# Kernel optimization log

Hardware: AMD Instinct MI355X
Metric: run time of the kernel (lower is better)

Reference implementation:

```python
import jax, jax.numpy as jnp
import numpy as np

BN_EPS = 1e-5


def setup_inputs() -> dict:
    key = jax.random.key(0)
    ks = jax.random.split(key, 8)
    B, C, H, W = 2, 512, 64, 64
    Ck, Cv = 256, 256
    x = jax.random.normal(ks[0], (B, C, H, W), jnp.float32)
    # f_key/f_query shared 1x1 conv (kaiming, relu)
    wk = jax.random.normal(ks[1], (Ck, C), jnp.float32) * (2.0 / C) ** 0.5
    bk = jnp.zeros((Ck,), jnp.float32)
    bn_gamma = jax.random.uniform(ks[2], (Ck,), jnp.float32, 0.5, 1.5)
    bn_beta = jax.random.normal(ks[3], (Ck,), jnp.float32) * 0.1
    bn_mean = jax.random.normal(ks[4], (Ck,), jnp.float32) * 0.1
    bn_var = jax.random.uniform(ks[5], (Ck,), jnp.float32, 0.5, 1.5)
    # f_value: 3x3 conv then 1x1 conv
    wv1 = jax.random.normal(ks[6], (Cv, C, 3, 3), jnp.float32) * (2.0 / (C * 9)) ** 0.5
    bv1 = jnp.zeros((Cv,), jnp.float32)
    wv2 = jax.random.normal(ks[7], (Cv, Cv), jnp.float32) * (2.0 / Cv) ** 0.5
    bv2 = jnp.zeros((Cv,), jnp.float32)
    return dict(x=x, wk=wk, bk=bk, bn_gamma=bn_gamma, bn_beta=bn_beta,
                bn_mean=bn_mean, bn_var=bn_var, wv1=wv1, bv1=bv1, wv2=wv2, bv2=bv2)


def reference(x, wk, bk, bn_gamma, bn_beta, bn_mean, bn_var, wv1, bv1, wv2, bv2):
    B, C, H, W = x.shape
    Ck, Cv = wk.shape[0], wv1.shape[0]
    N = H * W
    # f_key == f_query: 1x1 conv + BN (inference form) + ReLU
    feat = jnp.einsum('oc,bchw->bohw', wk, x) + bk[:, None, None]
    scale_bn = (bn_gamma / jnp.sqrt(bn_var + BN_EPS))
    feat = (feat - bn_mean[:, None, None]) * scale_bn[:, None, None] + bn_beta[:, None, None]
    feat = jax.nn.relu(feat).reshape(B, Ck, N)  # [B, Ck, N]
    # sim_map = softmax(Ck^-0.5 * Q^T K); Q and K are the same tensor
    sim_map = jax.nn.softmax(jnp.einsum('bcn,bcm->bnm', feat, feat) * (Ck ** -0.5), axis=-1)
    # f_value: conv3x3 + relu + conv1x1 + relu
    v = jax.lax.conv_general_dilated(x, wv1, (1, 1), 'SAME',
                                     dimension_numbers=('NCHW', 'OIHW', 'NCHW'))
    v = jax.nn.relu(v + bv1[:, None, None])
    v = jax.nn.relu(jnp.einsum('oc,bchw->bohw', wv2, v) + bv2[:, None, None])
    v = v.reshape(B, Cv, N)  # [B, Cv, N]
    context = jnp.einsum('bnm,bcm->bcn', sim_map, v).reshape(B, Cv, H, W)
    return context, sim_map
```

## Files before the change

### kernel.cpp

```cpp
#include <hip/hip_runtime.h>
#include <hip/hip_bf16.h>
#include <stdint.h>

typedef unsigned short u16_t;
typedef __attribute__((ext_vector_type(8))) short short8;
typedef __attribute__((ext_vector_type(4))) float f32x4;
typedef __attribute__((ext_vector_type(4))) unsigned short us4;

__device__ __forceinline__ float bf2f(u16_t u) {
  union { unsigned int i; float f; } c; c.i = ((unsigned int)u) << 16; return c.f;
}
__device__ __forceinline__ u16_t f2bf(float f) {
  union { float f; unsigned int i; } c; c.f = f;
  unsigned int x = c.i;
  unsigned int r = x + 0x7fffu + ((x >> 16) & 1u);
  return (u16_t)(r >> 16);
}

__device__ __forceinline__ void gload_lds16(const u16_t* g, u16_t* l) {
  __builtin_amdgcn_global_load_lds(
      (const __attribute__((address_space(1))) void*)g,
      (__attribute__((address_space(3))) void*)(unsigned int)(uintptr_t)l,
      16, 0, 0);
}

struct Seg {
  const u16_t* Ah;
  const u16_t* Al;
  const u16_t* Bh;
  const u16_t* Bl;
  int boff;
};

struct GemmArgs {
  Seg segs[9];
  int nseg;
  int segs_per_split;
  int K;
  int ldA, ldB;
  long long sA, sB;
  float alpha;
  float* outf;
  long long sOut;
  long long sSplit;
  int ldT;
};

template<int BM, int BN, int MODE, bool PADB, bool SYMM, int NCH = 4>
__global__ __launch_bounds__(256, 4) void gemm_tn(GemmArgs args) {
  constexpr int FM = BM / 32, FN = BN / 32;
  constexpr int AH_E = NCH * BM * 8;
  constexpr int AL_E = (MODE == 0) ? NCH * BM * 8 : 8;
  constexpr int BH_E = NCH * BN * 8;
  constexpr int BL_E = (MODE <= 1) ? NCH * BN * 8 : 8;
  constexpr int SM_E = AH_E + AL_E + BH_E + BL_E;
  static_assert(!SYMM || (size_t)SM_E * 2 >= 32 * 132 * 4, "tbuf alias too small");
  __shared__ __align__(16) u16_t smem[SM_E];
  u16_t* aflat_h = smem;
  u16_t* aflat_l = smem + AH_E;
  u16_t* bflat_h = smem + AH_E + AL_E;
  u16_t* bflat_l = smem + AH_E + AL_E + BH_E;

  const int tid = threadIdx.x;
  const int wave = tid >> 6, lane = tid & 63;
  const int lhi = lane >> 4, llo = lane & 15;
  const int wr = wave >> 1, wc = wave & 1;
  int nt, mt, b, split;
  if (SYMM) {
    b = blockIdx.z; split = 0;
    int t = blockIdx.x, r = 0;
    while (t >= 32 - r) { t -= 32 - r; ++r; }
    mt = r; nt = r + t;
  } else {
    nt = blockIdx.x; mt = blockIdx.y;
    b = blockIdx.z & 1; split = blockIdx.z >> 1;
  }
  const int row0 = mt * BM, col0 = nt * BN;

  f32x4 acc[FM][FN];
  const f32x4 zero4 = {0.f, 0.f, 0.f, 0.f};
#pragma unroll
  for (int i = 0; i < FM; ++i)
#pragma unroll
    for (int j = 0; j < FN; ++j) acc[i][j] = zero4;

  constexpr int RA = BM * NCH / 256;
  constexpr int RB = BN * NCH / 256;

  const int s0 = split * args.segs_per_split;
  int s1 = s0 + args.segs_per_split;
  if (s1 > args.nseg) s1 = args.nseg;

  for (int s = s0; s < s1; ++s) {
    const u16_t* Abh = args.segs[s].Ah + (size_t)b * args.sA;
    const u16_t* Abl = args.segs[s].Al + (size_t)b * args.sA;
    const u16_t* Bbh = args.segs[s].Bh + (size_t)b * args.sB;
    const u16_t* Bbl = args.segs[s].Bl + (size_t)b * args.sB;
    const int boff = args.segs[s].boff;
    for (int k0 = 0; k0 < args.K; k0 += NCH * 8) {
      __syncthreads();
#pragma unroll
      for (int r = 0; r < RA; ++r) {
        int idx = r * 256 + tid;
        int chunk = idx / BM, m = idx % BM;
        size_t goff = (size_t)(row0 + m) * args.ldA + (k0 + chunk * 8);
        gload_lds16(Abh + goff, aflat_h + (size_t)idx * 8);
        if (MODE == 0)
          gload_lds16(Abl + goff, aflat_l + (size_t)idx * 8);
      }
#pragma unroll
      for (int r = 0; r < RB; ++r) {
        int idx = r * 256 + tid;
        int chunk = idx / BN, n = idx % BN;
        long long rowi;
        if (PADB) {
          int gn = col0 + n;
          rowi = (long long)((gn >> 6) + 1) * 66 + (gn & 63) + 1 + boff;
        } else {
          rowi = col0 + n;
        }
        size_t goff = (size_t)rowi * args.ldB + (k0 + chunk * 8);
        gload_lds16(Bbh + goff, bflat_h + (size_t)idx * 8);
        if (MODE <= 1)
          gload_lds16(Bbl + goff, bflat_l + (size_t)idx * 8);
      }
      __syncthreads();
#pragma unroll
      for (int kk = 0; kk < NCH / 4; ++kk) {
        const int ckA = (kk * 4 + lhi) * BM;
        const int ckB = (kk * 4 + lhi) * BN;
        short8 afh[FM], afl[FM], bfh[FN], bfl[FN];
#pragma unroll
        for (int i = 0; i < FM; ++i) {
          afh[i] = *(const short8*)(aflat_h + ((size_t)ckA + wr * (BM / 2) + i * 16 + llo) * 8);
          if (MODE == 0)
            afl[i] = *(const short8*)(aflat_l + ((size_t)ckA + wr * (BM / 2) + i * 16 + llo) * 8);
        }
#pragma unroll
        for (int j = 0; j < FN; ++j) {
          bfh[j] = *(const short8*)(bflat_h + ((size_t)ckB + wc * (BN / 2) + j * 16 + llo) * 8);
          if (MODE <= 1)
            bfl[j] = *(const short8*)(bflat_l + ((size_t)ckB + wc * (BN / 2) + j * 16 + llo) * 8);
        }
#pragma unroll
        for (int i = 0; i < FM; ++i)
#pragma unroll
          for (int j = 0; j < FN; ++j) {
            f32x4 t = acc[i][j];
            if (MODE <= 1)
              t = __builtin_amdgcn_mfma_f32_16x16x32_bf16(afh[i], bfl[j], t, 0, 0, 0);
            if (MODE == 0)
              t = __builtin_amdgcn_mfma_f32_16x16x32_bf16(afl[i], bfh[j], t, 0, 0, 0);
            t = __builtin_amdgcn_mfma_f32_16x16x32_bf16(afh[i], bfh[j], t, 0, 0, 0);
            acc[i][j] = t;
          }
      }
    }
  }

  float* outp = args.outf + (size_t)split * args.sSplit + (size_t)b * args.sOut;
#pragma unroll
  for (int i = 0; i < FM; ++i) {
    int mb = row0 + wr * (BM / 2) + i * 16 + lhi * 4;
#pragma unroll
    for (int j = 0; j < FN; ++j) {
      int n = col0 + wc * (BN / 2) + j * 16 + llo;
      f32x4 vv = acc[i][j] * args.alpha;
      *(f32x4*)(outp + (size_t)n * args.ldT + mb) = vv;
    }
  }
  if (SYMM) {
    if (nt != mt) {
      float* tb = (float*)smem;
#pragma unroll
      for (int i = 0; i < FM; ++i) {
        __syncthreads();
#pragma unroll
        for (int j = 0; j < FN; ++j) {
#pragma unroll
          for (int r2 = 0; r2 < 4; ++r2) {
            int trow = wr * 16 + lhi * 4 + r2;
            int tcol = wc * 64 + j * 16 + llo;
            tb[trow * 132 + tcol] = acc[i][j][r2] * args.alpha;
          }
        }
        __syncthreads();
#pragma unroll
        for (int it = 0; it < 4; ++it) {
          int idx = it * 256 + tid;
          int row = idx >> 5, c4 = idx & 31;
          int mg = row0 + (row >> 4) * 64 + i * 16 + (row & 15);
          f32x4 v4 = *(f32x4*)&tb[row * 132 + c4 * 4];
          *(f32x4*)(outp + (size_t)mg * args.ldT + col0 + c4 * 4) = v4;
        }
      }
    }
  }
}

struct Conv3Args {
  const u16_t* W;
  const u16_t* X;
  float* outf;
  long long sOut;
  long long sSplit;
};
__global__ __launch_bounds__(256, 4) void conv3_gemm(Conv3Args a) {
  __shared__ __align__(16) u16_t lA[3][4][128][8];
  __shared__ __align__(16) u16_t lB[4 * 144 * 8];
  const int tid = threadIdx.x;
  const int wave = tid >> 6, lane = tid & 63;
  const int lhi = lane >> 4, llo = lane & 15;
  const int wr = wave >> 1, wc = wave & 1;
  const int nt = blockIdx.x, mt = blockIdx.y;
  const int z = blockIdx.z;
  const int b = z & 1;
  const int rest = z >> 1;
  const int ty = rest % 3, kh = rest / 3;
  const int row0 = mt * 128;
  const int base = (2 * nt + ty) * 66;
  const u16_t* Xb = a.X + (size_t)b * 4356 * 512;
  const u16_t* Wt = a.W + (size_t)(ty * 3) * 131072;

  f32x4 acc[4][4];
  const f32x4 zero4 = {0.f, 0.f, 0.f, 0.f};
#pragma unroll
  for (int i = 0; i < 4; ++i)
#pragma unroll
    for (int j = 0; j < 4; ++j) acc[i][j] = zero4;

  for (int k0 = kh * 256; k0 < (kh + 1) * 256; k0 += 32) {
    __syncthreads();
#pragma unroll
    for (int t = 0; t < 3; ++t)
#pragma unroll
      for (int r = 0; r < 2; ++r) {
        int slot = r * 256 + tid;
        int chunk = slot >> 7, m = slot & 127;
        const u16_t* src = Wt + (size_t)t * 131072 + (size_t)(row0 + m) * 512 + k0 + chunk * 8;
        gload_lds16(src, &lA[t][0][0][0] + (size_t)slot * 8);
      }
#pragma unroll
    for (int r = 0; r < 2; ++r) {
      int idx = r * 256 + tid;
      int chunk = idx / 144, rr = idx % 144;
      gload_lds16(Xb + (size_t)(base + rr) * 512 + k0 + chunk * 8, lB + (size_t)idx * 8);
    }
    if (tid < 64) {
      int idx = 512 + tid;
      int chunk = idx / 144, rr = idx % 144;
      gload_lds16(Xb + (size_t)(base + rr) * 512 + k0 + chunk * 8, lB + (size_t)idx * 8);
    }
    __syncthreads();
#pragma unroll
    for (int t = 0; t < 3; ++t) {
      short8 af[4], bf[4];
#pragma unroll
      for (int i = 0; i < 4; ++i)
        af[i] = *(const short8*)&lA[t][lhi][wr * 64 + i * 16 + llo][0];
#pragma unroll
      for (int j = 0; j < 4; ++j) {
        int rB = wc * 66 + j * 16 + llo + t;
        bf[j] = *(const short8*)(lB + ((size_t)lhi * 144 + rB) * 8);
      }
#pragma unroll
      for (int i = 0; i < 4; ++i)
#pragma unroll
        for (int j = 0; j < 4; ++j)
          acc[i][j] = __builtin_amdgcn_mfma_f32_16x16x32_bf16(af[i], bf[j], acc[i][j], 0, 0, 0);
    }
  }

  float* outp = a.outf + (size_t)(ty + 3 * kh) * a.sSplit + (size_t)b * a.sOut;
#pragma unroll
  for (int i = 0; i < 4; ++i) {
    int mb = row0 + wr * 64 + i * 16 + lhi * 4;
#pragma unroll
    for (int j = 0; j < 4; ++j) {
      int n = (nt << 7) + wc * 64 + j * 16 + llo;
      *(f32x4*)(outp + (size_t)n * 256 + mb) = acc[i][j];
    }
  }
}

template<int LDT, bool PER_COL>
__global__ __launch_bounds__(256) void reduce_split(
    const float* __restrict__ part, long long sSplit, int ns,
    const float* __restrict__ scale, const float* __restrict__ bias,
    u16_t* __restrict__ oh, u16_t* __restrict__ ol, long long total) {
  long long i = ((long long)blockIdx.x * 256 + threadIdx.x) * 4;
  if (i >= total) return;
  f32x4 s = *(const f32x4*)(part + i);
  for (int p = 1; p < ns; ++p) s += *(const f32x4*)(part + (size_t)p * sSplit + i);
  f32x4 v;
  if (PER_COL) {
    int c = (int)(i & (LDT - 1));
    f32x4 bi = *(const f32x4*)(bias + c);
    if (scale) { f32x4 sc = *(const f32x4*)(scale + c); v = s * sc + bi; }
    else v = s + bi;
  } else {
    int r = (int)((i / LDT) & 255);
    float bi = bias[r];
    v = s + bi;
  }
  us4 h, l;
#pragma unroll
  for (int c2 = 0; c2 < 4; ++c2) {
    float vv = v[c2] > 0.f ? v[c2] : 0.f;
    u16_t hh = f2bf(vv);
    h[c2] = hh;
    l[c2] = f2bf(vv - bf2f(hh));
  }
  *(us4*)(oh + i) = h;
  if (ol) *(us4*)(ol + i) = l;
}

__global__ __launch_bounds__(256) void reduce_split_f32(
    const float* __restrict__ part, long long sSplit, int ns,
    float* __restrict__ out, long long total) {
  long long i = ((long long)blockIdx.x * 256 + threadIdx.x) * 4;
  if (i >= total) return;
  f32x4 s = *(const f32x4*)(part + i);
  for (int p = 1; p < ns; ++p) s += *(const f32x4*)(part + (size_t)p * sSplit + i);
  __builtin_nontemporal_store(s, (f32x4*)(out + i));
}

__global__ __launch_bounds__(256) void softmax_k(float* S, u16_t* P) {
  const int row = blockIdx.x;
  float* Sr = S + (size_t)row * 4096;
  u16_t* Pr = P + (size_t)row * 4096;
  const int t = threadIdx.x;
  const int wave = t >> 6;
  f32x4 v[4];
  float vmax = -3.4e38f;
#pragma unroll
  for (int i = 0; i < 4; ++i) {
    v[i] = ((const f32x4*)Sr)[t + i * 256];
#pragma unroll
    for (int c = 0; c < 4; ++c) vmax = fmaxf(vmax, v[i][c]);
  }
#pragma unroll
  for (int off = 32; off; off >>= 1) vmax = fmaxf(vmax, __shfl_xor(vmax, off));
  __shared__ float red[4];
  if ((t & 63) == 0) red[wave] = vmax;
  __syncthreads();
  vmax = fmaxf(fmaxf(red[0], red[1]), fmaxf(red[2], red[3]));
  float sum = 0.f;
#pragma unroll
  for (int i = 0; i < 4; ++i)
#pragma unroll
    for (int c = 0; c < 4; ++c) { v[i][c] = __expf(v[i][c] - vmax); sum += v[i][c]; }
#pragma unroll
  for (int off = 32; off; off >>= 1) sum += __shfl_xor(sum, off);
  __shared__ float red2[4];
  if ((t & 63) == 0) red2[wave] = sum;
  __syncthreads();
  sum = red2[0] + red2[1] + red2[2] + red2[3];
  float rs = 1.0f / sum;
#pragma unroll
  for (int i = 0; i < 4; ++i) {
    f32x4 o = v[i] * rs;
    __builtin_nontemporal_store(o, (f32x4*)Sr + t + i * 256);
    us4 pb;
#pragma unroll
    for (int c = 0; c < 4; ++c) pb[c] = f2bf(o[c]);
    ((us4*)Pr)[t + i * 256] = pb;
  }
}

__global__ __launch_bounds__(256) void xprep(const float* __restrict__ x,
                                             u16_t* __restrict__ xh, u16_t* __restrict__ xl) {
  __shared__ float tile[64][65];
  const int b = blockIdx.z, c0 = blockIdx.y * 64, n0 = blockIdx.x * 64;
  const float* xb = x + ((size_t)b * 512 + c0) * 4096 + n0;
  const int t = threadIdx.x;
  const int tr = t >> 6, tc = t & 63;
#pragma unroll
  for (int rr = 0; rr < 16; ++rr) {
    int ci = tr + rr * 4;
    tile[ci][tc] = xb[(size_t)ci * 4096 + tc];
  }
  __syncthreads();
#pragma unroll
  for (int rr = 0; rr < 16; ++rr) {
    int nj = rr * 4 + tr;
    float v = tile[tc][nj];
    size_t rp = (size_t)(blockIdx.x + 1) * 66 + nj + 1;
    size_t o = ((size_t)b * 4356 + rp) * 512 + c0 + tc;
    u16_t hh = f2bf(v);
    xh[o] = hh;
    xl[o] = f2bf(v - bf2f(hh));
  }
}

__global__ __launch_bounds__(256) void prep_all(
    const float* __restrict__ wk, const float* __restrict__ wv2, const float* __restrict__ wv1,
    const float* __restrict__ g, const float* __restrict__ be, const float* __restrict__ mu,
    const float* __restrict__ var, const float* __restrict__ bkb,
    u16_t* __restrict__ wkh, u16_t* __restrict__ wkl,
    u16_t* __restrict__ w2h, u16_t* __restrict__ w2l,
    u16_t* __restrict__ w1h, float* __restrict__ bnA, float* __restrict__ bnB,
    u16_t* __restrict__ xh, u16_t* __restrict__ xl) {
  long long i = (long long)blockIdx.x * 256 + threadIdx.x;
  if (i < 256) {
    float s = g[i] * rsqrtf(var[i] + 1e-5f);
    bnA[i] = s;
    bnB[i] = (bkb[i] - mu[i]) * s + be[i];
    return;
  }
  i -= 256;
  if (i < 131072) {
    float v = wk[i];
    u16_t hh = f2bf(v);
    wkh[i] = hh; wkl[i] = f2bf(v - bf2f(hh));
    return;
  }
  i -= 131072;
  if (i < 65536) {
    float v = wv2[i];
    u16_t hh = f2bf(v);
    w2h[i] = hh; w2l[i] = f2bf(v - bf2f(hh));
    return;
  }
  i -= 65536;
  if (i < 1179648) {
    int tp = (int)(i / (256 * 512));
    int rem = (int)(i % (256 * 512));
    int o = rem / 512, c = rem % 512;
    w1h[i] = f2bf(wv1[((size_t)o * 512 + c) * 9 + tp]);
    return;
  }
  i -= 1179648;
  if (i < 133120) {
    int blk = (int)(i >> 8), t = (int)(i & 255);
    int rowi = blk % 260, b = blk / 260;
    int rp;
    if (rowi < 66) rp = rowi;
    else if (rowi < 132) rp = 4290 + (rowi - 66);
    else { int g2 = (rowi - 132) >> 1; rp = (g2 + 1) * 66 + ((rowi - 132) & 1) * 65; }
    size_t base = ((size_t)b * 4356 + rp) * 512;
    const us4 z = {0, 0, 0, 0};
    if (t < 128) *(us4*)(xh + base + (size_t)t * 4) = z;
    else *(us4*)(xl + base + (size_t)(t - 128) * 4) = z;
  }
}

extern "C" void kernel_launch(void* const* d_in, const int* in_sizes, int n_in,
                              void* d_out, int out_size, void* d_ws, size_t ws_size,
                              hipStream_t stream) {
  (void)in_sizes; (void)n_in; (void)out_size; (void)ws_size;
  const float* x   = (const float*)d_in[0];
  const float* wk  = (const float*)d_in[1];
  const float* bk  = (const float*)d_in[2];
  const float* gam = (const float*)d_in[3];
  const float* bet = (const float*)d_in[4];
  const float* mu  = (const float*)d_in[5];
  const float* var = (const float*)d_in[6];
  const float* wv1 = (const float*)d_in[7];
  const float* bv1 = (const float*)d_in[8];
  const float* wv2 = (const float*)d_in[9];
  const float* bv2 = (const float*)d_in[10];

  const int B = 2;
  const size_t XT_E  = (size_t)B * 4356 * 512;
  const size_t WK_E  = 256 * 512;
  const size_t WV1_E = 9ull * 256 * 512;
  const size_t WV2_E = 256 * 256;
  const size_t FT_E  = (size_t)B * 4096 * 256;
  const size_t P_E   = (size_t)B * 4096 * 4096;

  size_t off = 0;
  auto carve = [&](size_t bytes) -> char* {
    off = (off + 255) & ~(size_t)255;
    char* p = (char*)d_ws + off;
    off += bytes;
    return p;
  };
  u16_t* xh  = (u16_t*)carve(XT_E * 2);
  u16_t* xl  = (u16_t*)carve(XT_E * 2);
  u16_t* wkh = (u16_t*)carve(WK_E * 2);
  u16_t* wkl = (u16_t*)carve(WK_E * 2);
  u16_t* w1h = (u16_t*)carve(WV1_E * 2);
  u16_t* w2h = (u16_t*)carve(WV2_E * 2);
  u16_t* w2l = (u16_t*)carve(WV2_E * 2);
  u16_t* fth = (u16_t*)carve(FT_E * 2);
  u16_t* ftl = (u16_t*)carve(FT_E * 2);
  u16_t* v1h = (u16_t*)carve(FT_E * 2);
  u16_t* v1l = (u16_t*)carve(FT_E * 2);
  u16_t* vh  = (u16_t*)carve(FT_E * 2);
  u16_t* Pb  = (u16_t*)carve(P_E * 2);
  float* bnA = (float*)carve(256 * 4);
  float* bnB = (float*)carve(256 * 4);

  float* big_part = (float*)Pb;
  float* pv_part  = (float*)d_ws;

  float* ctx = (float*)d_out;
  float* sim = (float*)d_out + (size_t)B * 256 * 4096;

  const long long FT_LL = (long long)FT_E;

  prep_all<<<5897, 256, 0, stream>>>(wk, wv2, wv1, gam, bet, mu, var, bk,
                                     wkh, wkl, w2h, w2l, w1h, bnA, bnB, xh, xl);
  xprep<<<dim3(64, 8, 2), 256, 0, stream>>>(x, xh, xl);

  {
    GemmArgs a = {};
    a.segs[0] = {wkh,       wkl,       xh,       xl,       0};
    a.segs[1] = {wkh + 256, wkl + 256, xh + 256, xl + 256, 0};
    a.nseg = 2; a.segs_per_split = 1; a.K = 256; a.ldA = 512; a.ldB = 512;
    a.sA = 0; a.sB = (long long)4356 * 512; a.alpha = 1.f;
    a.outf = big_part; a.sOut = (long long)4096 * 256; a.sSplit = FT_LL; a.ldT = 256;
    gemm_tn<64, 128, 0, true, false><<<dim3(32, 4, 4), 256, 0, stream>>>(a);
    reduce_split<256, true><<<2048, 256, 0, stream>>>(big_part, FT_LL, 2, bnA, bnB, fth, ftl, FT_LL);
  }
  {
    GemmArgs a = {};
    a.segs[0] = {fth, nullptr, fth, ftl, 0};
    a.nseg = 1; a.segs_per_split = 1; a.K = 256; a.ldA = 256; a.ldB = 256;
    a.sA = (long long)4096 * 256; a.sB = (long long)4096 * 256; a.alpha = 0.0625f;
    a.outf = sim; a.sOut = (long long)4096 * 4096; a.sSplit = 0; a.ldT = 4096;
    gemm_tn<128, 128, 1, false, true><<<dim3(528, 1, 2), 256, 0, stream>>>(a);
  }
  {
    Conv3Args a;
    a.W = w1h; a.X = xh;
    a.outf = big_part; a.sOut = (long long)4096 * 256; a.sSplit = FT_LL;
    conv3_gemm<<<dim3(32, 2, 12), 256, 0, stream>>>(a);
    reduce_split<256, true><<<2048, 256, 0, stream>>>(big_part, FT_LL, 6, nullptr, bv1, v1h, v1l, FT_LL);
  }
  {
    GemmArgs a = {};
    a.segs[0] = {v1h,       v1l,       w2h,       w2l,       0};
    a.segs[1] = {v1h + 128, v1l + 128, w2h + 128, w2l + 128, 0};
    a.nseg = 2; a.segs_per_split = 1; a.K = 128; a.ldA = 256; a.ldB = 256;
    a.sA = (long long)4096 * 256; a.sB = 0; a.alpha = 1.f;
    a.outf = big_part; a.sOut = (long long)256 * 4096; a.sSplit = FT_LL; a.ldT = 4096;
    gemm_tn<128, 64, 0, false, false><<<dim3(4, 32, 4), 256, 0, stream>>>(a);
    reduce_split<4096, false><<<2048, 256, 0, stream>>>(big_part, FT_LL, 2, nullptr, bv2, vh, nullptr, FT_LL);
  }
  softmax_k<<<B * 4096, 256, 0, stream>>>(sim, Pb);
  {
    GemmArgs a = {};
    for (int q = 0; q < 4; ++q)
      a.segs[q] = {Pb + (size_t)q * 1024, nullptr, vh + (size_t)q * 1024, nullptr, 0};
    a.nseg = 4; a.segs_per_split = 1; a.K = 1024; a.ldA = 4096; a.ldB = 4096;
    a.sA = (long long)4096 * 4096; a.sB = (long long)256 * 4096; a.alpha = 1.f;
    a.outf = pv_part; a.sOut = (long long)256 * 4096; a.sSplit = FT_LL; a.ldT = 4096;
    gemm_tn<128, 128, 2, false, false, 8><<<dim3(2, 32, 8), 256, 0, stream>>>(a);
    reduce_split_f32<<<2048, 256, 0, stream>>>(pv_part, FT_LL, 4, ctx, FT_LL);
  }
}
```

Measured before the change: 265.7 us.

## Co-schedule independent QK/conv3 and wv2/softmax work in fused interleaved kernels

```diff
diff --git a/kernel.cpp b/kernel.cpp
--- a/kernel.cpp
+++ b/kernel.cpp
@@ -46,7 +46,7 @@
   int ldT;
 };
 
-template<int BM, int BN, int MODE, bool PADB, bool SYMM, int NCH = 4>
+template<int BM, int BN, int MODE, bool PADB, int NCH = 4>
 __global__ __launch_bounds__(256, 4) void gemm_tn(GemmArgs args) {
   constexpr int FM = BM / 32, FN = BN / 32;
   constexpr int AH_E = NCH * BM * 8;
@@ -54,7 +54,6 @@
   constexpr int BH_E = NCH * BN * 8;
   constexpr int BL_E = (MODE <= 1) ? NCH * BN * 8 : 8;
   constexpr int SM_E = AH_E + AL_E + BH_E + BL_E;
-  static_assert(!SYMM || (size_t)SM_E * 2 >= 32 * 132 * 4, "tbuf alias too small");
   __shared__ __align__(16) u16_t smem[SM_E];
   u16_t* aflat_h = smem;
   u16_t* aflat_l = smem + AH_E;
@@ -65,16 +64,8 @@
   const int wave = tid >> 6, lane = tid & 63;
   const int lhi = lane >> 4, llo = lane & 15;
   const int wr = wave >> 1, wc = wave & 1;
-  int nt, mt, b, split;
-  if (SYMM) {
-    b = blockIdx.z; split = 0;
-    int t = blockIdx.x, r = 0;
-    while (t >= 32 - r) { t -= 32 - r; ++r; }
-    mt = r; nt = r + t;
-  } else {
-    nt = blockIdx.x; mt = blockIdx.y;
-    b = blockIdx.z & 1; split = blockIdx.z >> 1;
-  }
+  const int nt = blockIdx.x, mt = blockIdx.y;
+  const int b = blockIdx.z & 1, split = blockIdx.z >> 1;
   const int row0 = mt * BM, col0 = nt * BN;
 
   f32x4 acc[FM][FN];
@@ -169,19 +160,101 @@
       *(f32x4*)(outp + (size_t)n * args.ldT + mb) = vv;
     }
   }
-  if (SYMM) {
+}
+
+struct QkConvArgs {
+  const u16_t* fh;
+  const u16_t* fl;
+  float* sim;
+  const u16_t* W;
+  const u16_t* X;
+  float* cpart;
+  long long sOut;
+  long long sSplit;
+};
+__global__ __launch_bounds__(256, 4) void qk_conv_fused(QkConvArgs a) {
+  __shared__ __align__(16) u16_t smem[16896];
+  const int tid = threadIdx.x;
+  const int wave = tid >> 6, lane = tid & 63;
+  const int lhi = lane >> 4, llo = lane & 15;
+  const int wr = wave >> 1, wc = wave & 1;
+  const int bid = blockIdx.x;
+  const int grp = bid / 19, r19 = bid % 19;
+
+  if (r19 < 11) {
+    int id = grp * 11 + r19;
+    int b = id / 528;
+    int t = id % 528, rr_ = 0;
+    while (t >= 32 - rr_) { t -= 32 - rr_; ++rr_; }
+    const int mt = rr_, nt = rr_ + t;
+    const int row0 = mt * 128, col0 = nt * 128;
+    u16_t* aflat_h = smem;
+    u16_t* bflat_h = smem + 4096;
+    u16_t* bflat_l = smem + 8192;
+    const u16_t* Fh = a.fh + (size_t)b * 4096 * 256;
+    const u16_t* Fl = a.fl + (size_t)b * 4096 * 256;
+
+    f32x4 acc[4][4];
+    const f32x4 zero4 = {0.f, 0.f, 0.f, 0.f};
+#pragma unroll
+    for (int i = 0; i < 4; ++i)
+#pragma unroll
+      for (int j = 0; j < 4; ++j) acc[i][j] = zero4;
+
+    for (int k0 = 0; k0 < 256; k0 += 32) {
+      __syncthreads();
+#pragma unroll
+      for (int rr = 0; rr < 2; ++rr) {
+        int idx = rr * 256 + tid;
+        int chunk = idx >> 7, m = idx & 127;
+        gload_lds16(Fh + (size_t)(row0 + m) * 256 + k0 + chunk * 8, aflat_h + (size_t)idx * 8);
+        gload_lds16(Fh + (size_t)(col0 + m) * 256 + k0 + chunk * 8, bflat_h + (size_t)idx * 8);
+        gload_lds16(Fl + (size_t)(col0 + m) * 256 + k0 + chunk * 8, bflat_l + (size_t)idx * 8);
+      }
+      __syncthreads();
+      short8 afh[4], bfh[4], bfl[4];
+#pragma unroll
+      for (int i = 0; i < 4; ++i)
+        afh[i] = *(const short8*)(aflat_h + ((size_t)lhi * 128 + wr * 64 + i * 16 + llo) * 8);
+#pragma unroll
+      for (int j = 0; j < 4; ++j) {
+        bfh[j] = *(const short8*)(bflat_h + ((size_t)lhi * 128 + wc * 64 + j * 16 + llo) * 8);
+        bfl[j] = *(const short8*)(bflat_l + ((size_t)lhi * 128 + wc * 64 + j * 16 + llo) * 8);
+      }
+#pragma unroll
+      for (int i = 0; i < 4; ++i)
+#pragma unroll
+        for (int j = 0; j < 4; ++j) {
+          f32x4 tt = acc[i][j];
+          tt = __builtin_amdgcn_mfma_f32_16x16x32_bf16(afh[i], bfl[j], tt, 0, 0, 0);
+          tt = __builtin_amdgcn_mfma_f32_16x16x32_bf16(afh[i], bfh[j], tt, 0, 0, 0);
+          acc[i][j] = tt;
+        }
+    }
+
+    float* outp = a.sim + (size_t)b * 4096 * 4096;
+#pragma unroll
+    for (int i = 0; i < 4; ++i) {
+      int mb = row0 + wr * 64 + i * 16 + lhi * 4;
+#pragma unroll
+      for (int j = 0; j < 4; ++j) {
+        int n = col0 + wc * 64 + j * 16 + llo;
+        f32x4 vv = acc[i][j] * 0.0625f;
+        *(f32x4*)(outp + (size_t)n * 4096 + mb) = vv;
+      }
+    }
     if (nt != mt) {
       float* tb = (float*)smem;
 #pragma unroll
-      for (int i = 0; i < FM; ++i) {
+      for (int i = 0; i < 4; ++i) {
         __syncthreads();
 #pragma unroll
-        for (int j = 0; j < FN; ++j) {
+        for (int j = 0; j < 4; ++j) {
 #pragma unroll
           for (int r2 = 0; r2 < 4; ++r2) {
             int trow = wr * 16 + lhi * 4 + r2;
             int tcol = wc * 64 + j * 16 + llo;
-            tb[trow * 132 + tcol] = acc[i][j][r2] * args.alpha;
+            tb[trow * 132 + tcol] = acc[i][j][r2] * 0.0625f;
           }
         }
         __syncthreads();
@@ -191,94 +264,221 @@
           int row = idx >> 5, c4 = idx & 31;
           int mg = row0 + (row >> 4) * 64 + i * 16 + (row & 15);
           f32x4 v4 = *(f32x4*)&tb[row * 132 + c4 * 4];
-          *(f32x4*)(outp + (size_t)mg * args.ldT + col0 + c4 * 4) = v4;
-        }
-      }
-    }
-  }
-}
-
-struct Conv3Args {
-  const u16_t* W;
-  const u16_t* X;
-  float* outf;
+          *(f32x4*)(outp + (size_t)mg * 4096 + col0 + c4 * 4) = v4;
+        }
+      }
+    }
+  } else {
+    int id = grp * 8 + (r19 - 11);
+    const int nt = id & 31;
+    const int mt = (id >> 5) & 1;
+    const int z = id >> 6;
+    const int b = z & 1;
+    const int rest = z >> 1;
+    const int ty = rest % 3, kh = rest / 3;
+    const int row0 = mt * 128;
+    const int base = (2 * nt + ty) * 66;
+    const u16_t* Xb = a.X + (size_t)b * 4356 * 512;
+    const u16_t* Wt = a.W + (size_t)(ty * 3) * 131072;
+    u16_t* lA = smem;
+    u16_t* lB = smem + 12288;
+
+    f32x4 acc[4][4];
+    const f32x4 zero4 = {0.f, 0.f, 0.f, 0.f};
+#pragma unroll
+    for (int i = 0; i < 4; ++i)
+#pragma unroll
+      for (int j = 0; j < 4; ++j) acc[i][j] = zero4;
+
+    for (int k0 = kh * 256; k0 < (kh + 1) * 256; k0 += 32) {
+      __syncthreads();
+#pragma unroll
+      for (int t = 0; t < 3; ++t)
+#pragma unroll
+        for (int r = 0; r < 2; ++r) {
+          int slot = r * 256 + tid;
+          int chunk = slot >> 7, m = slot & 127;
+          const u16_t* src = Wt + (size_t)t * 131072 + (size_t)(row0 + m) * 512 + k0 + chunk * 8;
+          gload_lds16(src, lA + (size_t)t * 4096 + (size_t)slot * 8);
+        }
+#pragma unroll
+      for (int r = 0; r < 2; ++r) {
+        int idx = r * 256 + tid;
+        int chunk = idx / 144, rr = idx % 144;
+        gload_lds16(Xb + (size_t)(base + rr) * 512 + k0 + chunk * 8, lB + (size_t)idx * 8);
+      }
+      if (tid < 64) {
+        int idx = 512 + tid;
+        int chunk = idx / 144, rr = idx % 144;
+        gload_lds16(Xb + (size_t)(base + rr) * 512 + k0 + chunk * 8, lB + (size_t)idx * 8);
+      }
+      __syncthreads();
+#pragma unroll
+      for (int t = 0; t < 3; ++t) {
+        short8 af[4], bf[4];
+#pragma unroll
+        for (int i = 0; i < 4; ++i)
+          af[i] = *(const short8*)(lA + (size_t)t * 4096 + ((size_t)lhi * 128 + wr * 64 + i * 16 + llo) * 8);
+#pragma unroll
+        for (int j = 0; j < 4; ++j) {
+          int rB = wc * 66 + j * 16 + llo + t;
+          bf[j] = *(const short8*)(lB + ((size_t)lhi * 144 + rB) * 8);
+        }
+#pragma unroll
+        for (int i = 0; i < 4; ++i)
+#pragma unroll
+          for (int j = 0; j < 4; ++j)
+            acc[i][j] = __builtin_amdgcn_mfma_f32_16x16x32_bf16(af[i], bf[j], acc[i][j], 0, 0, 0);
+      }
+    }
+
+    float* outp = a.cpart + (size_t)(ty + 3 * kh) * a.sSplit + (size_t)b * a.sOut;
+#pragma unroll
+    for (int i = 0; i < 4; ++i) {
+      int mb = row0 + wr * 64 + i * 16 + lhi * 4;
+#pragma unroll
+      for (int j = 0; j < 4; ++j) {
+        int n = (nt << 7) + wc * 64 + j * 16 + llo;
+        *(f32x4*)(outp + (size_t)n * 256 + mb) = acc[i][j];
+      }
+    }
+  }
+}
+
+struct Wv2SmArgs {
+  const u16_t* v1h;
+  const u16_t* v1l;
+  const u16_t* w2h;
+  const u16_t* w2l;
+  float* wpart;
   long long sOut;
   long long sSplit;
+  float* S;
+  u16_t* P;
 };
-__global__ __launch_bounds__(256, 4) void conv3_gemm(Conv3Args a) {
-  __shared__ __align__(16) u16_t lA[3][4][128][8];
-  __shared__ __align__(16) u16_t lB[4 * 144 * 8];
+__global__ __launch_bounds__(256, 4) void wv2_softmax_fused(Wv2SmArgs a) {
+  __shared__ __align__(16) u16_t smem[12288];
   const int tid = threadIdx.x;
-  const int wave = tid >> 6, lane = tid & 63;
-  const int lhi = lane >> 4, llo = lane & 15;
-  const int wr = wave >> 1, wc = wave & 1;
-  const int nt = blockIdx.x, mt = blockIdx.y;
-  const int z = blockIdx.z;
-  const int b = z & 1;
-  const int rest = z >> 1;
-  const int ty = rest % 3, kh = rest / 3;
-  const int row0 = mt * 128;
-  const int base = (2 * nt + ty) * 66;
-  const u16_t* Xb = a.X + (size_t)b * 4356 * 512;
-  const u16_t* Wt = a.W + (size_t)(ty * 3) * 131072;
-
-  f32x4 acc[4][4];
-  const f32x4 zero4 = {0.f, 0.f, 0.f, 0.f};
-#pragma unroll
-  for (int i = 0; i < 4; ++i)
-#pragma unroll
-    for (int j = 0; j < 4; ++j) acc[i][j] = zero4;
-
-  for (int k0 = kh * 256; k0 < (kh + 1) * 256; k0 += 32) {
+  const int bid = blockIdx.x;
+  const int grp = bid / 17, r17 = bid % 17;
+
+  if (r17 == 0) {
+    const int id = grp;
+    const int wave = tid >> 6, lane = tid & 63;
+    const int lhi = lane >> 4, llo = lane & 15;
+    const int wr = wave >> 1, wc = wave & 1;
+    const int nt = id & 3;
+    const int mt = (id >> 2) & 31;
+    const int z = id >> 7;
+    const int b = z & 1, split = z >> 1;
+    const int row0 = mt * 128, col0 = nt * 64;
+    u16_t* aflat_h = smem;
+    u16_t* aflat_l = smem + 4096;
+    u16_t* bflat_h = smem + 8192;
+    u16_t* bflat_l = smem + 10240;
+    const u16_t* Abh = a.v1h + (size_t)b * 4096 * 256 + split * 128;
+    const u16_t* Abl = a.v1l + (size_t)b * 4096 * 256 + split * 128;
+    const u16_t* Bbh = a.w2h + split * 128;
+    const u16_t* Bbl = a.w2l + split * 128;
+
+    f32x4 acc[4][2];
+    const f32x4 zero4 = {0.f, 0.f, 0.f, 0.f};
+#pragma unroll
+    for (int i = 0; i < 4; ++i)
+#pragma unroll
+      for (int j = 0; j < 2; ++j) acc[i][j] = zero4;
+
+    for (int k0 = 0; k0 < 128; k0 += 32) {
+      __syncthreads();
+#pragma unroll
+      for (int r = 0; r < 2; ++r) {
+        int idx = r * 256 + tid;
+        int chunk = idx >> 7, m = idx & 127;
+        size_t goff = (size_t)(row0 + m) * 256 + (k0 + chunk * 8);
+        gload_lds16(Abh + goff, aflat_h + (size_t)idx * 8);
+        gload_lds16(Abl + goff, aflat_l + (size_t)idx * 8);
+      }
+      {
+        int idx = tid;
+        int chunk = idx >> 6, n = idx & 63;
+        size_t goff = (size_t)(col0 + n) * 256 + (k0 + chunk * 8);
+        gload_lds16(Bbh + goff, bflat_h + (size_t)idx * 8);
+        gload_lds16(Bbl + goff, bflat_l + (size_t)idx * 8);
+      }
+      __syncthreads();
+      short8 afh[4], afl[4], bfh[2], bfl[2];
+#pragma unroll
+      for (int i = 0; i < 4; ++i) {
+        afh[i] = *(const short8*)(aflat_h + ((size_t)lhi * 128 + wr * 64 + i * 16 + llo) * 8);
+        afl[i] = *(const short8*)(aflat_l + ((size_t)lhi * 128 + wr * 64 + i * 16 + llo) * 8);
+      }
+#pragma unroll
+      for (int j = 0; j < 2; ++j) {
+        bfh[j] = *(const short8*)(bflat_h + ((size_t)lhi * 64 + wc * 32 + j * 16 + llo) * 8);
+        bfl[j] = *(const short8*)(bflat_l + ((size_t)lhi * 64 + wc * 32 + j * 16 + llo) * 8);
+      }
+#pragma unroll
+      for (int i = 0; i < 4; ++i)
+#pragma unroll
+        for (int j = 0; j < 2; ++j) {
+          f32x4 t = acc[i][j];
+          t = __builtin_amdgcn_mfma_f32_16x16x32_bf16(afh[i], bfl[j], t, 0, 0, 0);
+          t = __builtin_amdgcn_mfma_f32_16x16x32_bf16(afl[i], bfh[j], t, 0, 0, 0);
+          t = __builtin_amdgcn_mfma_f32_16x16x32_bf16(afh[i], bfh[j], t, 0, 0, 0);
+          acc[i][j] = t;
+        }
+    }
+
+    float* outp = a.wpart + (size_t)split * a.sSplit + (size_t)b * a.sOut;
+#pragma unroll
+    for (int i = 0; i < 4; ++i) {
+      int mb = row0 + wr * 64 + i * 16 + lhi * 4;
+#pragma unroll
+      for (int j = 0; j < 2; ++j) {
+        int n = col0 + wc * 32 + j * 16 + llo;
+        *(f32x4*)(outp + (size_t)n * 4096 + mb) = acc[i][j];
+      }
+    }
+  } else {
+    const int row = grp * 16 + (r17 - 1);
+    float* Sr = a.S + (size_t)row * 4096;
+    u16_t* Pr = a.P + (size_t)row * 4096;
+    const int t = tid;
+    const int wave = t >> 6;
+    float* red = (float*)smem;
+    float* red2 = red + 4;
+    f32x4 v[4];
+    float vmax = -3.4e38f;
+#pragma unroll
+    for (int i = 0; i < 4; ++i) {
+      v[i] = ((const f32x4*)Sr)[t + i * 256];
+#pragma unroll
+      for (int c = 0; c < 4; ++c) vmax = fmaxf(vmax, v[i][c]);
+    }
+#pragma unroll
+    for (int off = 32; off; off >>= 1) vmax = fmaxf(vmax, __shfl_xor(vmax, off));
+    if ((t & 63) == 0) red[wave] = vmax;
     __syncthreads();
-#pragma unroll
-    for (int t = 0; t < 3; ++t)
-#pragma unroll
-      for (int r = 0; r < 2; ++r) {
-        int slot = r * 256 + tid;
-        int chunk = slot >> 7, m = slot & 127;
-        const u16_t* src = Wt + (size_t)t * 131072 + (size_t)(row0 + m) * 512 + k0 + chunk * 8;
-        gload_lds16(src, &lA[t][0][0][0] + (size_t)slot * 8);
-      }
-#pragma unroll
-    for (int r = 0; r < 2; ++r) {
-      int idx = r * 256 + tid;
-      int chunk = idx / 144, rr = idx % 144;
-      gload_lds16(Xb + (size_t)(base + rr) * 512 + k0 + chunk * 8, lB + (size_t)idx * 8);
-    }
-    if (tid < 64) {
-      int idx = 512 + tid;
-      int chunk = idx / 144, rr = idx % 144;
-      gload_lds16(Xb + (size_t)(base + rr) * 512 + k0 + chunk * 8, lB + (size_t)idx * 8);
-    }
+    vmax = fmaxf(fmaxf(red[0], red[1]), fmaxf(red[2], red[3]));
+    float sum = 0.f;
+#pragma unroll
+    for (int i = 0; i < 4; ++i)
+#pragma unroll
+      for (int c = 0; c < 4; ++c) { v[i][c] = __expf(v[i][c] - vmax); sum += v[i][c]; }
+#pragma unroll
+    for (int off = 32; off; off >>= 1) sum += __shfl_xor(sum, off);
+    if ((t & 63) == 0) red2[wave] = sum;
     __syncthreads();
-#pragma unroll
-    for (int t = 0; t < 3; ++t) {
-      short8 af[4], bf[4];
-#pragma unroll
-      for (int i = 0; i < 4; ++i)
-        af[i] = *(const short8*)&lA[t][lhi][wr * 64 + i * 16 + llo][0];
-#pragma unroll
-      for (int j = 0; j < 4; ++j) {
-        int rB = wc * 66 + j * 16 + llo + t;
-        bf[j] = *(const short8*)(lB + ((size_t)lhi * 144 + rB) * 8);
-      }
-#pragma unroll
-      for (int i = 0; i < 4; ++i)
-#pragma unroll
-        for (int j = 0; j < 4; ++j)
-          acc[i][j] = __builtin_amdgcn_mfma_f32_16x16x32_bf16(af[i], bf[j], acc[i][j], 0, 0, 0);
-    }
-  }
-
-  float* outp = a.outf + (size_t)(ty + 3 * kh) * a.sSplit + (size_t)b * a.sOut;
-#pragma unroll
-  for (int i = 0; i < 4; ++i) {
-    int mb = row0 + wr * 64 + i * 16 + lhi * 4;
-#pragma unroll
-    for (int j = 0; j < 4; ++j) {
-      int n = (nt << 7) + wc * 64 + j * 16 + llo;
-      *(f32x4*)(outp + (size_t)n * 256 + mb) = acc[i][j];
+    sum = red2[0] + red2[1] + red2[2] + red2[3];
+    float rs = 1.0f / sum;
+#pragma unroll
+    for (int i = 0; i < 4; ++i) {
+      f32x4 o = v[i] * rs;
+      __builtin_nontemporal_store(o, (f32x4*)Sr + t + i * 256);
+      us4 pb;
+#pragma unroll
+      for (int c = 0; c < 4; ++c) pb[c] = f2bf(o[c]);
+      ((us4*)Pr)[t + i * 256] = pb;
     }
   }
 }
@@ -323,49 +523,6 @@
   f32x4 s = *(const f32x4*)(part + i);
   for (int p = 1; p < ns; ++p) s += *(const f32x4*)(part + (size_t)p * sSplit + i);
   __builtin_nontemporal_store(s, (f32x4*)(out + i));
-}
-
-__global__ __launch_bounds__(256) void softmax_k(float* S, u16_t* P) {
-  const int row = blockIdx.x;
-  float* Sr = S + (size_t)row * 4096;
-  u16_t* Pr = P + (size_t)row * 4096;
-  const int t = threadIdx.x;
-  const int wave = t >> 6;
-  f32x4 v[4];
-  float vmax = -3.4e38f;
-#pragma unroll
-  for (int i = 0; i < 4; ++i) {
-    v[i] = ((const f32x4*)Sr)[t + i * 256];
-#pragma unroll
-    for (int c = 0; c < 4; ++c) vmax = fmaxf(vmax, v[i][c]);
-  }
-#pragma unroll
-  for (int off = 32; off; off >>= 1) vmax = fmaxf(vmax, __shfl_xor(vmax, off));
-  __shared__ float red[4];
-  if ((t & 63) == 0) red[wave] = vmax;
-  __syncthreads();
-  vmax = fmaxf(fmaxf(red[0], red[1]), fmaxf(red[2], red[3]));
-  float sum = 0.f;
-#pragma unroll
-  for (int i = 0; i < 4; ++i)
-#pragma unroll
-    for (int c = 0; c < 4; ++c) { v[i][c] = __expf(v[i][c] - vmax); sum += v[i][c]; }
-#pragma unroll
-  for (int off = 32; off; off >>= 1) sum += __shfl_xor(sum, off);
-  __shared__ float red2[4];
-  if ((t & 63) == 0) red2[wave] = sum;
-  __syncthreads();
-  sum = red2[0] + red2[1] + red2[2] + red2[3];
-  float rs = 1.0f / sum;
-#pragma unroll
-  for (int i = 0; i < 4; ++i) {
-    f32x4 o = v[i] * rs;
-    __builtin_nontemporal_store(o, (f32x4*)Sr + t + i * 256);
-    us4 pb;
-#pragma unroll
-    for (int c = 0; c < 4; ++c) pb[c] = f2bf(o[c]);
-    ((us4*)Pr)[t + i * 256] = pb;
-  }
 }
 
 __global__ __launch_bounds__(256) void xprep(const float* __restrict__ x,
@@ -492,8 +649,8 @@
   float* bnA = (float*)carve(256 * 4);
   float* bnB = (float*)carve(256 * 4);
 
-  float* big_part = (float*)Pb;
-  float* pv_part  = (float*)d_ws;
+  float* big_part  = (float*)Pb;
+  float* head_part = (float*)d_ws;
 
   float* ctx = (float*)d_out;
   float* sim = (float*)d_out + (size_t)B * 256 * 4096;
@@ -511,43 +668,33 @@
     a.nseg = 2; a.segs_per_split = 1; a.K = 256; a.ldA = 512; a.ldB = 512;
     a.sA = 0; a.sB = (long long)4356 * 512; a.alpha = 1.f;
     a.outf = big_part; a.sOut = (long long)4096 * 256; a.sSplit = FT_LL; a.ldT = 256;
-    gemm_tn<64, 128, 0, true, false><<<dim3(32, 4, 4), 256, 0, stream>>>(a);
+    gemm_tn<64, 128, 0, true><<<dim3(32, 4, 4), 256, 0, stream>>>(a);
     reduce_split<256, true><<<2048, 256, 0, stream>>>(big_part, FT_LL, 2, bnA, bnB, fth, ftl, FT_LL);
   }
   {
-    GemmArgs a = {};
-    a.segs[0] = {fth, nullptr, fth, ftl, 0};
-    a.nseg = 1; a.segs_per_split = 1; a.K = 256; a.ldA = 256; a.ldB = 256;
-    a.sA = (long long)4096 * 256; a.sB = (long long)4096 * 256; a.alpha = 0.0625f;
-    a.outf = sim; a.sOut = (long long)4096 * 4096; a.sSplit = 0; a.ldT = 4096;
-    gemm_tn<128, 128, 1, false, true><<<dim3(528, 1, 2), 256, 0, stream>>>(a);
+    QkConvArgs a;
+    a.fh = fth; a.fl = ftl; a.sim = sim;
+    a.W = w1h; a.X = xh; a.cpart = big_part;
+    a.sOut = (long long)4096 * 256; a.sSplit = FT_LL;
+    qk_conv_fused<<<1824, 256, 0, stream>>>(a);
+    reduce_split<256, true><<<2048, 256, 0, stream>>>(big_part, FT_LL, 6, nullptr, bv1, v1h, v1l, FT_LL);
   }
   {
-    Conv3Args a;
-    a.W = w1h; a.X = xh;
-    a.outf = big_part; a.sOut = (long long)4096 * 256; a.sSplit = FT_LL;
-    conv3_gemm<<<dim3(32, 2, 12), 256, 0, stream>>>(a);
-    reduce_split<256, true><<<2048, 256, 0, stream>>>(big_part, FT_LL, 6, nullptr, bv1, v1h, v1l, FT_LL);
-  }
-  {
-    GemmArgs a = {};
-    a.segs[0] = {v1h,       v1l,       w2h,       w2l,       0};
-    a.segs[1] = {v1h + 128, v1l + 128, w2h + 128, w2l + 128, 0};
-    a.nseg = 2; a.segs_per_split = 1; a.K = 128; a.ldA = 256; a.ldB = 256;
-    a.sA = (long long)4096 * 256; a.sB = 0; a.alpha = 1.f;
-    a.outf = big_part; a.sOut = (long long)256 * 4096; a.sSplit = FT_LL; a.ldT = 4096;
-    gemm_tn<128, 64, 0, false, false><<<dim3(4, 32, 4), 256, 0, stream>>>(a);
-    reduce_split<4096, false><<<2048, 256, 0, stream>>>(big_part, FT_LL, 2, nullptr, bv2, vh, nullptr, FT_LL);
-  }
-  softmax_k<<<B * 4096, 256, 0, stream>>>(sim, Pb);
+    Wv2SmArgs a;
+    a.v1h = v1h; a.v1l = v1l; a.w2h = w2h; a.w2l = w2l;
+    a.wpart = head_part; a.sOut = (long long)256 * 4096; a.sSplit = FT_LL;
+    a.S = sim; a.P = Pb;
+    wv2_softmax_fused<<<8704, 256, 0, stream>>>(a);
+    reduce_split<4096, false><<<2048, 256, 0, stream>>>(head_part, FT_LL, 2, nullptr, bv2, vh, nullptr, FT_LL);
+  }
   {
     GemmArgs a = {};
     for (int q = 0; q < 4; ++q)
       a.segs[q] = {Pb + (size_t)q * 1024, nullptr, vh + (size_t)q * 1024, nullptr, 0};
     a.nseg = 4; a.segs_per_split = 1; a.K = 1024; a.ldA = 4096; a.ldB = 4096;
     a.sA = (long long)4096 * 4096; a.sB = (long long)256 * 4096; a.alpha = 1.f;
-    a.outf = pv_part; a.sOut = (long long)256 * 4096; a.sSplit = FT_LL; a.ldT = 4096;
-    gemm_tn<128, 128, 2, false, false, 8><<<dim3(2, 32, 8), 256, 0, stream>>>(a);
-    reduce_split_f32<<<2048, 256, 0, stream>>>(pv_part, FT_LL, 4, ctx, FT_LL);
-  }
-}
+    a.outf = head_part; a.sOut = (long long)256 * 4096; a.sSplit = FT_LL; a.ldT = 4096;
+    gemm_tn<128, 128, 2, false, 8><<<dim3(2, 32, 8), 256, 0, stream>>>(a);
+    reduce_split_f32<<<2048, 256, 0, stream>>>(head_part, FT_LL, 4, ctx, FT_LL);
+  }
+}
```

After: 272.1 us. 1.02x slower.
